# Kernel optimization log

Measured on AMD Instinct MI355X. Metric: run time of the kernel, lower is better.

The kernel has to match this reference:

```python
import jax, jax.numpy as jnp
import numpy as np

B, T, H, V = 16, 400, 400, 22000
S, STEPS, NG = 30, 8, 3  # n_slots, max_res_len, n_gates


def setup_inputs() -> dict:
    key = jax.random.key(0)
    ks = jax.random.split(key, 12)
    r = lambda k, shape, s: jax.random.normal(k, shape, jnp.float32) * s
    lens = jnp.sort(jax.random.randint(ks[8], (B,), T // 2, T + 1))[::-1]
    lens = lens.at[0].set(T)  # torch code only masks up to max(lens); make max(lens)==T
    return {
        "embedding": r(ks[0], (V, H), 0.1),
        "gru_Wih": r(ks[1], (3 * H, H), 0.05),
        "gru_Whh": r(ks[2], (3 * H, H), 0.05),
        "gru_bih": jnp.zeros((3 * H,), jnp.float32),
        "gru_bhh": jnp.zeros((3 * H,), jnp.float32),
        "W_ratio": r(ks[3], (1, 3 * H), 0.05),
        "b_ratio": jnp.zeros((1,), jnp.float32),
        "W_gate": r(ks[4], (NG, H), 0.05),
        "b_gate": jnp.zeros((NG,), jnp.float32),
        "slot_embs": r(ks[5], (S, H), 0.1),  # domain_emb + slot_emb, precombined per domain-slot
        "encoded_hidden": r(ks[6], (B, H), 1.0),
        "encoded_outputs": r(ks[7], (B, T, H), 1.0),
        "encoded_lens": lens,
        "story": jax.random.randint(ks[9], (B, T), 0, V),
        "target_batches": jax.random.randint(ks[10], (B, S, STEPS), 0, V),
    }


def reference(embedding, gru_Wih, gru_Whh, gru_bih, gru_bhh, W_ratio, b_ratio,
              W_gate, b_gate, slot_embs, encoded_hidden, encoded_outputs,
              encoded_lens, story, target_batches):
    # dropout is identity at eval; use_teacher_forcing=True.
    mask = jnp.arange(T)[None, :] < encoded_lens[:, None]          # [B, T]
    batch_idx = jnp.arange(B)[:, None]

    def gru_cell(x, h):
        gi = x @ gru_Wih.T + gru_bih                                # [B, 3H]
        gh = h @ gru_Whh.T + gru_bhh
        i_r, i_z, i_n = jnp.split(gi, 3, axis=-1)
        h_r, h_z, h_n = jnp.split(gh, 3, axis=-1)
        r = jax.nn.sigmoid(i_r + h_r)
        z = jax.nn.sigmoid(i_z + h_z)
        n = jnp.tanh(i_n + r * h_n)
        return (1.0 - z) * n + z * h

    def per_slot(slot_emb, tgt_steps):  # slot_emb [H], tgt_steps [STEPS, B]
        dec_in0 = jnp.broadcast_to(slot_emb[None, :], (B, H))

        def step(carry, tgt_w):
            h, dec_in = carry
            h = gru_cell(dec_in, h)                                 # dec_state == new hidden
            logits = jnp.einsum('bth,bh->bt', encoded_outputs, h)   # [B, T]
            attn = jax.nn.softmax(jnp.where(mask, logits, -1e9), axis=1)
            context = jnp.einsum('bt,bth->bh', attn, encoded_outputs)
            p_vocab = jax.nn.softmax(h @ embedding.T, axis=1)       # [B, V]
            pg_in = jnp.concatenate([h, context, dec_in], axis=-1)  # [B, 3H]
            p_gen = jax.nn.sigmoid(pg_in @ W_ratio.T + b_ratio)     # [B, 1]
            p_ctx = jnp.zeros((B, V), p_vocab.dtype).at[batch_idx, story].add(attn)
            p_final = (1.0 - p_gen) * p_ctx + p_gen * p_vocab       # [B, V]
            dec_next = embedding[tgt_w]                             # teacher forcing
            return (h, dec_next), (p_final, context)

        _, (points, contexts) = jax.lax.scan(step, (encoded_hidden, dec_in0), tgt_steps)
        gate = contexts[0] @ W_gate.T + b_gate                      # gate uses step-0 context
        return jnp.transpose(points, (1, 0, 2)), gate               # [B, STEPS, V], [B, NG]

    targets = jnp.transpose(target_batches, (1, 2, 0))              # [S, STEPS, B]
    all_point_outputs, all_gate_outputs = jax.vmap(per_slot)(slot_embs, targets)
    return all_point_outputs, all_gate_outputs  # [S,B,STEPS,V], [S,B,NG]
```

## Files before the change

kernel.cpp:

```cpp
#include <hip/hip_runtime.h>
#include <hip/hip_bf16.h>

#define DEV __device__ __forceinline__

constexpr int B = 16, T = 400, H = 400, V = 22000, S = 30, STEPS = 8, NG = 3;
constexpr int M  = S * B;
constexpr int H3 = 3 * H;
constexpr int KP = 416;
constexpr int VP = 22016;
constexpr int MP = 512;
constexpr int MR = STEPS * MP;
constexpr int NWP = 1280;
constexpr int NBLK = VP / 128;
constexpr int NMP = MR / 256;
constexpr int NVB = NBLK * NMP;
constexpr int TPAD = 416;
constexpr int PLD = 424;
constexpr long long PTS = (long long)S * B * STEPS * V;

typedef __attribute__((ext_vector_type(8))) short bfrag;
typedef __attribute__((ext_vector_type(4))) float f32x4;
typedef unsigned short u16;

DEV u16 f2bf(float x) {
  unsigned u = __float_as_uint(x);
  u += 0x7FFFu + ((u >> 16) & 1u);
  return (u16)(u >> 16);
}
DEV u16 f2bfn(float x) {
  __hip_bfloat16 h = __float2bfloat16(x);
  union { __hip_bfloat16 b; u16 u; } cv; cv.b = h; return cv.u;
}
DEV float bf2f(u16 h) { return __uint_as_float(((unsigned)h) << 16); }
DEV float sigm(float x) { return 1.0f / (1.0f + __expf(-x)); }

DEV void gload16(const u16* g, u16* l) {
  __builtin_amdgcn_global_load_lds(
      (const __attribute__((address_space(1))) void*)g,
      (__attribute__((address_space(3))) void*)l, 16, 0, 0);
}

constexpr int N_EMB = VP * KP / 256;
constexpr int N_ENC = B * 400 * TPAD / 256;
constexpr int N_W   = NWP * KP / 256;
constexpr int N_DEC = STEPS * MP * KP / 256;
constexpr int N_H0  = MP * KP / 256;
constexpr int N_ZP  = STEPS * (MP - M) * KP / 256;
constexpr int N_ZE  = MR * 16 / 256;
constexpr int N_INIT = N_EMB + N_ENC + N_W + N_DEC + N_H0 + N_ZP + N_ZE;

__global__ __launch_bounds__(256) void k_init(
    const float* __restrict__ emb, const float* __restrict__ enc,
    const float* __restrict__ Wih, const float* __restrict__ Whh,
    const float* __restrict__ semb, const float* __restrict__ ehid,
    const int* __restrict__ tgt,
    u16* __restrict__ ebf, u16* __restrict__ encbK, u16* __restrict__ encT,
    u16* __restrict__ wihH, u16* __restrict__ wihL,
    u16* __restrict__ whhH, u16* __restrict__ whhL,
    float* __restrict__ dec, u16* __restrict__ decH, u16* __restrict__ decL,
    float* __restrict__ h0F, u16* __restrict__ h0H, u16* __restrict__ h0L,
    u16* __restrict__ hAllH, u16* __restrict__ hAllL, u16* __restrict__ ebuf)
{
  int bx = blockIdx.x;
  const int tid = threadIdx.x;
  if (bx < N_EMB) {
    int i = bx * 256 + tid;
    int v = i / KP, k = i % KP;
    ebf[i] = f2bf((v < V && k < H) ? emb[(long long)v * H + k] : 0.f);
    return;
  }
  bx -= N_EMB;
  if (bx < N_ENC) {
    int i = bx * 256 + tid;
    int c = i % TPAD, r = (i / TPAD) % 400, b = i / (TPAD * 400);
    encbK[i] = f2bf((c < H) ? enc[((size_t)b * T + r) * H + c] : 0.f);
    encT[i]  = f2bf((c < T) ? enc[((size_t)b * T + c) * H + r] : 0.f);
    return;
  }
  bx -= N_ENC;
  if (bx < N_W) {
    int i = bx * 256 + tid;
    int n = i / KP, k = i % KP;
    float v1 = (n < H3 && k < H) ? Wih[n * H + k] : 0.f;
    u16 h1 = f2bf(v1);
    wihH[i] = h1; wihL[i] = f2bf(v1 - bf2f(h1));
    float v2 = (n < H3 && k < H) ? Whh[n * H + k] : 0.f;
    u16 h2 = f2bf(v2);
    whhH[i] = h2; whhL[i] = f2bf(v2 - bf2f(h2));
    return;
  }
  bx -= N_W;
  if (bx < N_DEC) {
    int i = bx * 256 + tid;
    int k = i % KP, m = (i / KP) % MP, s = i / (KP * MP);
    float val = 0.f;
    if (m < M && k < H) {
      int slot = m / B, b = m % B;
      if (s == 0) val = semb[slot * H + k];
      else        val = emb[(long long)tgt[(b * S + slot) * STEPS + (s - 1)] * H + k];
      dec[((long long)s * M + m) * H + k] = val;
    }
    u16 hi = f2bf(val);
    decH[i] = hi; decL[i] = f2bf(val - bf2f(hi));
    return;
  }
  bx -= N_DEC;
  if (bx < N_H0) {
    int i = bx * 256 + tid;
    int k = i % KP, m = i / KP;
    float val = (m < M && k < H) ? ehid[(m % B) * H + k] : 0.f;
    if (m < M && k < H) h0F[m * H + k] = val;
    u16 hi = f2bf(val);
    h0H[i] = hi; h0L[i] = f2bf(val - bf2f(hi));
    return;
  }
  bx -= N_H0;
  if (bx < N_ZP) {
    int i = bx * 256 + tid;
    int k = i % KP;
    int row = M + (i / KP) % (MP - M);
    int s = i / (KP * (MP - M));
    size_t idx = ((size_t)s * MP + row) * KP + k;
    hAllH[idx] = 0; hAllL[idx] = 0;
    return;
  }
  bx -= N_ZP;
  {
    int i = bx * 256 + tid;
    int row = i / 16, col = V + (i % 16);
    ebuf[(size_t)row * VP + col] = 0;
  }
}

__global__ __launch_bounds__(256) void k_gemm64s(
    const u16* __restrict__ Ahi, const u16* __restrict__ Alo,
    const u16* __restrict__ Bmh, const u16* __restrict__ Bml,
    const float* __restrict__ bias, float* __restrict__ C,
    int Mvalid, int Nvalid, int Cstride)
{
  __shared__ u16 BsH[64 * 32], BsL[64 * 32];
  const int tid = threadIdx.x;
  const int wave = tid >> 6, lane = tid & 63;
  const int wm = wave >> 1, wn = wave & 1;
  const int n0 = blockIdx.x * 64;
  const int m0 = blockIdx.y * 64;
  const int lrow = lane & 15;
  const int c16 = lane >> 4;
  const int srow = tid >> 2;
  const int sg = (tid & 3) ^ (srow & 3);
  f32x4 acc[2][2] = {};

  const u16* aH = Ahi + (size_t)(m0 + wm * 32 + lrow) * KP + c16 * 8;
  const u16* aL = Alo + (size_t)(m0 + wm * 32 + lrow) * KP + c16 * 8;
  const u16* bHs = Bmh + (size_t)(n0 + srow) * KP + sg * 8;
  const u16* bLs = Bml + (size_t)(n0 + srow) * KP + sg * 8;
  u16* lBH = BsH + wave * 512;
  u16* lBL = BsL + wave * 512;

  for (int kk = 0; kk < KP / 32; ++kk) {
    const int kb = kk * 32;
    gload16(bHs + kb, lBH);
    gload16(bLs + kb, lBL);
    __syncthreads();
    bfrag a0h = *(const bfrag*)(aH + kb);
    bfrag a1h = *(const bfrag*)(aH + 16 * KP + kb);
    bfrag a0l = *(const bfrag*)(aL + kb);
    bfrag a1l = *(const bfrag*)(aL + 16 * KP + kb);
#pragma unroll
    for (int nn = 0; nn < 2; ++nn) {
      const int br = wn * 32 + nn * 16 + lrow;
      const int goff = br * 32 + ((c16 ^ (br & 3)) << 3);
      bfrag bh = *(const bfrag*)&BsH[goff];
      bfrag bl = *(const bfrag*)&BsL[goff];
      acc[0][nn] = __builtin_amdgcn_mfma_f32_16x16x32_bf16(a0h, bh, acc[0][nn], 0, 0, 0);
      acc[1][nn] = __builtin_amdgcn_mfma_f32_16x16x32_bf16(a1h, bh, acc[1][nn], 0, 0, 0);
      acc[0][nn] = __builtin_amdgcn_mfma_f32_16x16x32_bf16(a0h, bl, acc[0][nn], 0, 0, 0);
      acc[1][nn] = __builtin_amdgcn_mfma_f32_16x16x32_bf16(a1h, bl, acc[1][nn], 0, 0, 0);
      acc[0][nn] = __builtin_amdgcn_mfma_f32_16x16x32_bf16(a0l, bh, acc[0][nn], 0, 0, 0);
      acc[1][nn] = __builtin_amdgcn_mfma_f32_16x16x32_bf16(a1l, bh, acc[1][nn], 0, 0, 0);
    }
    __syncthreads();
  }
  const int orow = (lane >> 4) << 2, ocol = lane & 15;
#pragma unroll
  for (int am = 0; am < 2; ++am) {
#pragma unroll
    for (int nn = 0; nn < 2; ++nn) {
      const int gn = n0 + wn * 32 + nn * 16 + ocol;
      if (gn >= Nvalid) continue;
      const float badd = bias[gn];
#pragma unroll
      for (int r = 0; r < 4; ++r) {
        const int gm = m0 + wm * 32 + am * 16 + orow + r;
        if (gm < Mvalid) C[(long long)gm * Cstride + gn] = acc[am][nn][r] + badd;
      }
    }
  }
}

__global__ __launch_bounds__(512) void k_cell(const float* __restrict__ gi_s,
                                              const float* __restrict__ gh,
                                              const float* __restrict__ hprevF,
                                              float* __restrict__ hcurF,
                                              u16* __restrict__ hHc, u16* __restrict__ hLc) {
  int i = blockIdx.x * 512 + threadIdx.x;
  if (i >= M * H) return;
  int k = i % H, m = i / H;
  float ir = gi_s[m * H3 + k],         hr = gh[m * H3 + k];
  float iz = gi_s[m * H3 + H + k],     hz = gh[m * H3 + H + k];
  float in_ = gi_s[m * H3 + 2*H + k],  hn = gh[m * H3 + 2*H + k];
  float rr = sigm(ir + hr);
  float z = sigm(iz + hz);
  float n = tanhf(in_ + rr * hn);
  float hv = (1.f - z) * n + z * hprevF[i];
  hcurF[i] = hv;
  u16 hb = f2bf(hv);
  hHc[m * KP + k] = hb;
  hLc[m * KP + k] = f2bf(hv - bf2f(hb));
}

struct SMatt {
  u16 P[32 * PLD];
  float partm[32][4];
  float parts[32][4];
  float rowred[32];
  float part2[32][4][4];
};

__global__ __launch_bounds__(512) void k_attn(
    const u16* __restrict__ hAllH, const u16* __restrict__ hAllL,
    const float* __restrict__ hallF,
    const u16* __restrict__ encbK, const u16* __restrict__ encT,
    const int* __restrict__ lens, const float* __restrict__ dec,
    const float* __restrict__ Wr, const float* __restrict__ br,
    const float* __restrict__ Wg, const float* __restrict__ bg,
    float* __restrict__ attnB, float* __restrict__ pgenB, float* __restrict__ out)
{
  __shared__ SMatt sm;
  const int s = blockIdx.x >> 4;
  const int b = blockIdx.x & 15;
  const int tid = threadIdx.x;
  const int wave = tid >> 6, lane = tid & 63;
  const int mt = wave & 1;
  const int wg = wave >> 1;
  const int lrow = lane & 15;
  const int c16 = lane >> 4;
  const int len = lens[b];
  const int rbase = mt * 16 + c16 * 4;

  for (int idx = tid; idx < 32 * 24; idx += 512)
    sm.P[(idx / 24) * PLD + 400 + (idx % 24)] = 0;

  f32x4 acc[7] = {};
  {
    const size_t arow = (size_t)s * MP + (size_t)(mt * 16 + lrow) * B + b;
    const u16* aHp = hAllH + arow * KP + c16 * 8;
    const u16* aLp = hAllL + arow * KP + c16 * 8;
    const u16* bBase = encbK + (size_t)b * 400 * TPAD + c16 * 8;
    for (int kk = 0; kk < 13; ++kk) {
      bfrag ah = *(const bfrag*)(aHp + kk * 32);
      bfrag al = *(const bfrag*)(aLp + kk * 32);
#pragma unroll
      for (int i = 0; i < 7; ++i) {
        const int jt = wg + 4 * i;
        if (jt < 25) {
          bfrag bv = *(const bfrag*)(bBase + (size_t)(jt * 16 + lrow) * TPAD + kk * 32);
          acc[i] = __builtin_amdgcn_mfma_f32_16x16x32_bf16(ah, bv, acc[i], 0, 0, 0);
          acc[i] = __builtin_amdgcn_mfma_f32_16x16x32_bf16(al, bv, acc[i], 0, 0, 0);
        }
      }
    }
  }

  {
    float pm[4] = {-1e30f, -1e30f, -1e30f, -1e30f};
#pragma unroll
    for (int i = 0; i < 7; ++i) {
      const int jt = wg + 4 * i;
      if (jt >= 25) continue;
      const int t = jt * 16 + lrow;
      const bool ok = t < len;
#pragma unroll
      for (int rr = 0; rr < 4; ++rr) pm[rr] = fmaxf(pm[rr], ok ? acc[i][rr] : -1e30f);
    }
#pragma unroll
    for (int d = 1; d < 16; d <<= 1) {
#pragma unroll
      for (int rr = 0; rr < 4; ++rr) pm[rr] = fmaxf(pm[rr], __shfl_xor(pm[rr], d));
    }
    if (lrow == 0) {
#pragma unroll
      for (int rr = 0; rr < 4; ++rr) sm.partm[rbase + rr][wg] = pm[rr];
    }
  }
  __syncthreads();
  if (tid < 32)
    sm.rowred[tid] = fmaxf(fmaxf(sm.partm[tid][0], sm.partm[tid][1]),
                           fmaxf(sm.partm[tid][2], sm.partm[tid][3]));
  __syncthreads();
  float Mx[4];
#pragma unroll
  for (int rr = 0; rr < 4; ++rr) Mx[rr] = sm.rowred[rbase + rr];
  {
    float ps[4] = {0.f, 0.f, 0.f, 0.f};
#pragma unroll
    for (int i = 0; i < 7; ++i) {
      const int jt = wg + 4 * i;
      if (jt >= 25) continue;
      const int t = jt * 16 + lrow;
      const bool ok = t < len;
#pragma unroll
      for (int rr = 0; rr < 4; ++rr) {
        float e = ok ? __expf(acc[i][rr] - Mx[rr]) : 0.f;
        acc[i][rr] = e;
        ps[rr] += e;
      }
    }
#pragma unroll
    for (int d = 1; d < 16; d <<= 1) {
#pragma unroll
      for (int rr = 0; rr < 4; ++rr) ps[rr] += __shfl_xor(ps[rr], d);
    }
    if (lrow == 0) {
#pragma unroll
      for (int rr = 0; rr < 4; ++rr) sm.parts[rbase + rr][wg] = ps[rr];
    }
  }
  __syncthreads();
  if (tid < 32)
    sm.rowred[tid] = sm.parts[tid][0] + sm.parts[tid][1] + sm.parts[tid][2] + sm.parts[tid][3];
  __syncthreads();
  {
    float inv[4];
#pragma unroll
    for (int rr = 0; rr < 4; ++rr) inv[rr] = 1.f / sm.rowred[rbase + rr];
#pragma unroll
    for (int i = 0; i < 7; ++i) {
      const int jt = wg + 4 * i;
      if (jt >= 25) continue;
      const int t = jt * 16 + lrow;
#pragma unroll
      for (int rr = 0; rr < 4; ++rr) {
        const int row = rbase + rr;
        const float p = acc[i][rr] * inv[rr];
        sm.P[row * PLD + t] = f2bfn(p);
        if (row < 30) attnB[((size_t)s * M + row * B + b) * T + t] = p;
      }
    }
  }
  __syncthreads();

  f32x4 acc2[7] = {};
  {
    const u16* bBase = encT + (size_t)b * 400 * TPAD + c16 * 8;
    const u16* aP = sm.P + (mt * 16 + lrow) * PLD + c16 * 8;
    for (int kk = 0; kk < 13; ++kk) {
      bfrag ap = *(const bfrag*)(aP + kk * 32);
#pragma unroll
      for (int i = 0; i < 7; ++i) {
        const int jk = wg + 4 * i;
        if (jk < 25) {
          bfrag bv = *(const bfrag*)(bBase + (size_t)(jk * 16 + lrow) * TPAD + kk * 32);
          acc2[i] = __builtin_amdgcn_mfma_f32_16x16x32_bf16(ap, bv, acc2[i], 0, 0, 0);
        }
      }
    }
  }
  {
    float pw[4] = {0.f, 0.f, 0.f, 0.f};
    float pg0[4] = {0.f, 0.f, 0.f, 0.f};
    float pg1[4] = {0.f, 0.f, 0.f, 0.f};
    float pg2[4] = {0.f, 0.f, 0.f, 0.f};
    const bool do_g = (s == 0);
#pragma unroll
    for (int i = 0; i < 7; ++i) {
      const int jk = wg + 4 * i;
      if (jk >= 25) continue;
      const int k = jk * 16 + lrow;
      const float wr = Wr[H + k];
      float w0 = 0.f, w1 = 0.f, w2 = 0.f;
      if (do_g) { w0 = Wg[k]; w1 = Wg[H + k]; w2 = Wg[2 * H + k]; }
#pragma unroll
      for (int rr = 0; rr < 4; ++rr) {
        const float v = acc2[i][rr];
        pw[rr] = fmaf(v, wr, pw[rr]);
        if (do_g) {
          pg0[rr] = fmaf(v, w0, pg0[rr]);
          pg1[rr] = fmaf(v, w1, pg1[rr]);
          pg2[rr] = fmaf(v, w2, pg2[rr]);
        }
      }
    }
#pragma unroll
    for (int d = 1; d < 16; d <<= 1) {
#pragma unroll
      for (int rr = 0; rr < 4; ++rr) {
        pw[rr] += __shfl_xor(pw[rr], d);
        pg0[rr] += __shfl_xor(pg0[rr], d);
        pg1[rr] += __shfl_xor(pg1[rr], d);
        pg2[rr] += __shfl_xor(pg2[rr], d);
      }
    }
    if (lrow == 0) {
#pragma unroll
      for (int rr = 0; rr < 4; ++rr) {
        sm.part2[rbase + rr][wg][0] = pw[rr];
        sm.part2[rbase + rr][wg][1] = pg0[rr];
        sm.part2[rbase + rr][wg][2] = pg1[rr];
        sm.part2[rbase + rr][wg][3] = pg2[rr];
      }
    }
  }
  __syncthreads();

  if (tid < 480) {
    const int row = tid >> 4;
    const int l16 = tid & 15;
    const int m = row * B + b;
    const float* hF = hallF + ((size_t)s * M + m) * H;
    const float* dF = dec + ((size_t)s * M + m) * H;
    float p = 0.f;
    for (int j = 0; j < 25; ++j) {
      const int k = l16 + 16 * j;
      p += hF[k] * Wr[k] + dF[k] * Wr[2 * H + k];
    }
#pragma unroll
    for (int d = 1; d < 16; d <<= 1) p += __shfl_xor(p, d);
    if (l16 == 0) {
      float cw = sm.part2[row][0][0] + sm.part2[row][1][0] +
                 sm.part2[row][2][0] + sm.part2[row][3][0];
      pgenB[s * M + m] = sigm(p + cw + br[0]);
    }
    if (s == 0 && l16 < NG) {
      float gv = sm.part2[row][0][1 + l16] + sm.part2[row][1][1 + l16] +
                 sm.part2[row][2][1 + l16] + sm.part2[row][3][1 + l16];
      out[PTS + (long long)m * NG + l16] = gv + bg[l16];
    }
  }
}

__global__ __launch_bounds__(512) void k_vocab(
    const u16* __restrict__ hAllH, const u16* __restrict__ ebf,
    u16* __restrict__ ebuf)
{
  __shared__ u16 Bs[4][4096];
  const int bx = blockIdx.x;
  const int tid = threadIdx.x;
  const int wave = tid >> 6, lane = tid & 63;
  const int bxs = (bx & 7) * (NVB / 8) + (bx >> 3);
  const int nb = bxs / NMP;
  const int mp = bxs % NMP;
  const int n0 = nb * 128;
  const int m0 = mp * 256;
  const int wm = wave >> 1, wn = wave & 1;
  const int lrow = lane & 15;
  const int c16 = lane >> 4;
  const int srow = tid >> 2;
  const int sg = (tid & 3) ^ (srow & 3);
  f32x4 acc[4][4] = {};

  const u16* aBase = hAllH + (size_t)(m0 + wm * 64 + lrow) * KP + c16 * 8;
  const u16* bS = ebf + (size_t)(n0 + srow) * KP + sg * 8;

  gload16(bS + 0,  &Bs[0][wave * 512]);
  gload16(bS + 32, &Bs[1][wave * 512]);
  int cur = 0;
#pragma unroll 1
  for (int p = 0; p < 7; ++p) {
    const int kb = p * 64;
    bfrag a[4][2];
#pragma unroll
    for (int r = 0; r < 4; ++r) {
      a[r][0] = *(const bfrag*)(aBase + r * 16 * KP + kb);
      if (p < 6) a[r][1] = *(const bfrag*)(aBase + r * 16 * KP + kb + 32);
    }
    if (p < 5) {
      gload16(bS + kb + 64, &Bs[(cur ^ 1) * 2 + 0][wave * 512]);
      gload16(bS + kb + 96, &Bs[(cur ^ 1) * 2 + 1][wave * 512]);
      asm volatile("s_waitcnt vmcnt(10)" ::: "memory");
    } else if (p == 5) {
      gload16(bS + kb + 64, &Bs[(cur ^ 1) * 2 + 0][wave * 512]);
      asm volatile("s_waitcnt vmcnt(9)" ::: "memory");
    } else {
      asm volatile("s_waitcnt vmcnt(4)" ::: "memory");
    }
    __builtin_amdgcn_sched_barrier(0);
    __builtin_amdgcn_s_barrier();
    {
      const u16* Bb = Bs[cur * 2 + 0];
      bfrag bfv[4];
#pragma unroll
      for (int nn = 0; nn < 4; ++nn) {
        const int brr = wn * 64 + nn * 16 + lrow;
        bfv[nn] = *(const bfrag*)&Bb[brr * 32 + ((c16 ^ (brr & 3)) << 3)];
      }
#pragma unroll
      for (int nn = 0; nn < 4; ++nn) {
#pragma unroll
        for (int r = 0; r < 4; ++r)
          acc[r][nn] = __builtin_amdgcn_mfma_f32_16x16x32_bf16(a[r][0], bfv[nn], acc[r][nn], 0, 0, 0);
      }
    }
    if (p < 6) {
      const u16* Bb = Bs[cur * 2 + 1];
      bfrag bfv[4];
#pragma unroll
      for (int nn = 0; nn < 4; ++nn) {
        const int brr = wn * 64 + nn * 16 + lrow;
        bfv[nn] = *(const bfrag*)&Bb[brr * 32 + ((c16 ^ (brr & 3)) << 3)];
      }
#pragma unroll
      for (int nn = 0; nn < 4; ++nn) {
#pragma unroll
        for (int r = 0; r < 4; ++r)
          acc[r][nn] = __builtin_amdgcn_mfma_f32_16x16x32_bf16(a[r][1], bfv[nn], acc[r][nn], 0, 0, 0);
      }
    }
    __builtin_amdgcn_sched_barrier(0);
    __builtin_amdgcn_s_barrier();
    __builtin_amdgcn_sched_barrier(0);
    cur ^= 1;
  }

  const int orow = (lane >> 4) << 2, ocol = lane & 15;
#pragma unroll
  for (int af = 0; af < 4; ++af) {
#pragma unroll
    for (int r = 0; r < 4; ++r) {
      const int rl = wm * 64 + af * 16 + orow + r;
      const size_t R = (size_t)m0 + rl;
      if ((R % MP) >= M) continue;
#pragma unroll
      for (int nn = 0; nn < 4; ++nn) {
        const int gn = n0 + wn * 64 + nn * 16 + ocol;
        if (gn < V) ebuf[R * VP + gn] = f2bfn(__expf(acc[af][nn][r]));
      }
    }
  }
}

__global__ __launch_bounds__(512) void k_merge(
    const u16* __restrict__ ebuf, const float* __restrict__ pgenB,
    const float* __restrict__ attnB, const int* __restrict__ story,
    float* __restrict__ out)
{
  const int bxi = blockIdx.x;
  const int s = bxi / M, m = bxi % M, b = m % B;
  const size_t R = (size_t)s * MP + m;
  const int tid = threadIdx.x;
  const int wave = tid >> 6, lane = tid & 63;
  __shared__ float red8[8];
  const u16* erow = ebuf + R * VP;
  bfrag ch[6];
  float sum = 0.f;
#pragma unroll
  for (int j = 0; j < 6; ++j) {
    const int c = j * 512 + tid;
    if (c < VP / 8) {
      ch[j] = *(const bfrag*)(erow + (size_t)c * 8);
#pragma unroll
      for (int e = 0; e < 8; ++e) sum += bf2f((u16)ch[j][e]);
    }
  }
#pragma unroll
  for (int off = 32; off; off >>= 1) sum += __shfl_xor(sum, off);
  if (lane == 0) red8[wave] = sum;
  __syncthreads();
  float Sv = 0.f;
#pragma unroll
  for (int j = 0; j < 8; ++j) Sv += red8[j];
  const float pg = pgenB[s * M + m];
  const float scale = pg / Sv;
  float* orow = out + ((size_t)m * STEPS + s) * V;
#pragma unroll
  for (int j = 0; j < 6; ++j) {
    const int c = j * 512 + tid;
    if (c < V / 8) {
      f32x4 w0, w1;
#pragma unroll
      for (int e = 0; e < 4; ++e) {
        w0[e] = bf2f((u16)ch[j][e]) * scale;
        w1[e] = bf2f((u16)ch[j][4 + e]) * scale;
      }
      *(f32x4*)(orow + (size_t)c * 8) = w0;
      *(f32x4*)(orow + (size_t)c * 8 + 4) = w1;
    }
  }
  __syncthreads();
  const float om = 1.f - pg;
  for (int t = tid; t < T; t += 512) {
    float a = attnB[((size_t)s * M + m) * T + t];
    if (a != 0.f) atomicAdd(orow + story[b * T + t], om * a);
  }
}


extern "C" void kernel_launch(void* const* d_in, const int* in_sizes, int n_in,
                              void* d_out, int out_size, void* d_ws, size_t ws_size,
                              hipStream_t stream) {
  (void)in_sizes; (void)n_in; (void)out_size; (void)ws_size;
  const float* emb  = (const float*)d_in[0];
  const float* Wih  = (const float*)d_in[1];
  const float* Whh  = (const float*)d_in[2];
  const float* bih  = (const float*)d_in[3];
  const float* bhh  = (const float*)d_in[4];
  const float* Wr   = (const float*)d_in[5];
  const float* br   = (const float*)d_in[6];
  const float* Wg   = (const float*)d_in[7];
  const float* bg   = (const float*)d_in[8];
  const float* semb = (const float*)d_in[9];
  const float* ehid = (const float*)d_in[10];
  const float* enc  = (const float*)d_in[11];
  const int*   lens = (const int*)d_in[12];
  const int*   story= (const int*)d_in[13];
  const int*   tgt  = (const int*)d_in[14];
  float* out = (float*)d_out;

  char* w = (char*)d_ws;
  size_t off = 0;
  auto alloc = [&](size_t n) -> void* {
    void* p = w + off;
    off = (off + n + 255) & ~(size_t)255;
    return p;
  };
  u16* ebf    = (u16*)alloc((size_t)VP * KP * 2);
  u16* wihH   = (u16*)alloc((size_t)NWP * KP * 2);
  u16* wihL   = (u16*)alloc((size_t)NWP * KP * 2);
  u16* whhH   = (u16*)alloc((size_t)NWP * KP * 2);
  u16* whhL   = (u16*)alloc((size_t)NWP * KP * 2);
  u16* decH   = (u16*)alloc((size_t)STEPS * MP * KP * 2);
  u16* decL   = (u16*)alloc((size_t)STEPS * MP * KP * 2);
  float* dec  = (float*)alloc((size_t)STEPS * M * H * 4);
  float* h0F  = (float*)alloc((size_t)M * H * 4);
  u16* h0H    = (u16*)alloc((size_t)MP * KP * 2);
  u16* h0L    = (u16*)alloc((size_t)MP * KP * 2);
  u16* hAllH  = (u16*)alloc((size_t)MR * KP * 2);
  u16* hAllL  = (u16*)alloc((size_t)MR * KP * 2);
  float* hallF= (float*)alloc((size_t)STEPS * M * H * 4);
  float* gi   = (float*)alloc((size_t)MR * H3 * 4);
  float* gh   = (float*)alloc((size_t)M * H3 * 4);
  float* attnB= (float*)alloc((size_t)STEPS * M * T * 4);
  float* pgenB= (float*)alloc((size_t)STEPS * M * 4);
  u16* ebuf   = (u16*)alloc((size_t)MR * VP * 2);
  u16* encbK  = (u16*)alloc((size_t)B * 400 * TPAD * 2);
  u16* encT   = (u16*)alloc((size_t)B * 400 * TPAD * 2);

  k_init<<<N_INIT, 256, 0, stream>>>(emb, enc, Wih, Whh, semb, ehid, tgt,
      ebf, encbK, encT, wihH, wihL, whhH, whhL, dec, decH, decL,
      h0F, h0H, h0L, hAllH, hAllL, ebuf);
  k_gemm64s<<<dim3((H3 + 63) / 64, MR / 64), 256, 0, stream>>>(
      decH, decL, wihH, wihL, bih, gi, MR, H3, H3);

  for (int s = 0; s < STEPS; ++s) {
    const u16* pH = (s == 0) ? h0H : hAllH + (size_t)(s - 1) * MP * KP;
    const u16* pL = (s == 0) ? h0L : hAllL + (size_t)(s - 1) * MP * KP;
    const float* pF = (s == 0) ? h0F : hallF + (size_t)(s - 1) * M * H;
    k_gemm64s<<<dim3((H3 + 63) / 64, (M + 63) / 64), 256, 0, stream>>>(
        pH, pL, whhH, whhL, bhh, gh, M, H3, H3);
    k_cell<<<(M * H + 511) / 512, 512, 0, stream>>>(
        gi + (size_t)s * MP * H3, gh, pF,
        hallF + (size_t)s * M * H,
        hAllH + (size_t)s * MP * KP, hAllL + (size_t)s * MP * KP);
  }

  k_vocab<<<NVB, 512, 0, stream>>>(hAllH, ebf, ebuf);
  k_attn<<<STEPS * B, 512, 0, stream>>>(hAllH, hAllL, hallF, encbK, encT, lens,
                                        dec, Wr, br, Wg, bg, attnB, pgenB, out);
  k_merge<<<STEPS * M, 512, 0, stream>>>(ebuf, pgenB, attnB, story, out);
}
```

Before: 605.1 us.

## Fuse per-step vocab GEMM with recurrent GEMM to overlap serial GRU chain

Splits the single large vocab-projection GEMM into per-step slices and launches each slice in the same kernel as the next step's recurrent h@Whh GEMM. Block index decides which role a block takes, so the vocab work fills the GPU while the small, latency-bound recurrent GEMM runs. This removes the separate vocab kernel at the end and hides it behind the sequential GRU loop. In exchange the recurrent GEMM now runs with 512-thread blocks of which half idle, and per-step vocab launches have smaller grids with less L2 reuse of the embedding matrix.

```diff
diff --git a/kernel.cpp b/kernel.cpp
--- a/kernel.cpp
+++ b/kernel.cpp
@@ -14,6 +14,9 @@
 constexpr int NBLK = VP / 128;
 constexpr int NMP = MR / 256;
 constexpr int NVB = NBLK * NMP;
+constexpr int NVB_S = NBLK * 2;
+constexpr int NCT = (H3 + 63) / 64;
+constexpr int NGH = NCT * ((M + 63) / 64);
 constexpr int TPAD = 416;
 constexpr int PLD = 424;
 constexpr long long PTS = (long long)S * B * STEPS * V;
@@ -217,6 +220,177 @@
   u16 hb = f2bf(hv);
   hHc[m * KP + k] = hb;
   hLc[m * KP + k] = f2bf(hv - bf2f(hb));
+}
+
+__global__ __launch_bounds__(512) void k_bigv(
+    const u16* __restrict__ hPrevH, const u16* __restrict__ hPrevL,
+    const u16* __restrict__ ebf, u16* __restrict__ ebuf, long long Rbase,
+    const u16* __restrict__ whhH, const u16* __restrict__ whhL,
+    const float* __restrict__ bhh, float* __restrict__ gh)
+{
+  __shared__ union SMU {
+    u16 vb[4][4096];
+    struct { u16 bh[64 * 32]; u16 bl[64 * 32]; } g;
+  } sm;
+  const int bx = blockIdx.x;
+  const int tid = threadIdx.x;
+  const int wave = tid >> 6, lane = tid & 63;
+
+  if (bx < NVB_S) {
+    const int bxs = (bx & 7) * (NVB_S / 8) + (bx >> 3);
+    const int nb = bxs >> 1;
+    const int m0 = (bxs & 1) * 256;
+    const int n0 = nb * 128;
+    const int wm = wave >> 1, wn = wave & 1;
+    const int lrow = lane & 15;
+    const int c16 = lane >> 4;
+    const int srow = tid >> 2;
+    const int sg = (tid & 3) ^ (srow & 3);
+    f32x4 acc[4][4] = {};
+
+    const u16* aBase = hPrevH + (size_t)(m0 + wm * 64 + lrow) * KP + c16 * 8;
+    const u16* bS = ebf + (size_t)(n0 + srow) * KP + sg * 8;
+
+    gload16(bS + 0,  &sm.vb[0][wave * 512]);
+    gload16(bS + 32, &sm.vb[1][wave * 512]);
+    int cur = 0;
+#pragma unroll 1
+    for (int p = 0; p < 7; ++p) {
+      const int kb = p * 64;
+      bfrag a[4][2];
+#pragma unroll
+      for (int r = 0; r < 4; ++r) {
+        a[r][0] = *(const bfrag*)(aBase + r * 16 * KP + kb);
+        if (p < 6) a[r][1] = *(const bfrag*)(aBase + r * 16 * KP + kb + 32);
+      }
+      if (p < 5) {
+        gload16(bS + kb + 64, &sm.vb[(cur ^ 1) * 2 + 0][wave * 512]);
+        gload16(bS + kb + 96, &sm.vb[(cur ^ 1) * 2 + 1][wave * 512]);
+        asm volatile("s_waitcnt vmcnt(10)" ::: "memory");
+      } else if (p == 5) {
+        gload16(bS + kb + 64, &sm.vb[(cur ^ 1) * 2 + 0][wave * 512]);
+        asm volatile("s_waitcnt vmcnt(9)" ::: "memory");
+      } else {
+        asm volatile("s_waitcnt vmcnt(4)" ::: "memory");
+      }
+      __builtin_amdgcn_sched_barrier(0);
+      __builtin_amdgcn_s_barrier();
+      {
+        const u16* Bb = sm.vb[cur * 2 + 0];
+        bfrag bfv[4];
+#pragma unroll
+        for (int nn = 0; nn < 4; ++nn) {
+          const int brr = wn * 64 + nn * 16 + lrow;
+          bfv[nn] = *(const bfrag*)&Bb[brr * 32 + ((c16 ^ (brr & 3)) << 3)];
+        }
+#pragma unroll
+        for (int nn = 0; nn < 4; ++nn) {
+#pragma unroll
+          for (int r = 0; r < 4; ++r)
+            acc[r][nn] = __builtin_amdgcn_mfma_f32_16x16x32_bf16(a[r][0], bfv[nn], acc[r][nn], 0, 0, 0);
+        }
+      }
+      if (p < 6) {
+        const u16* Bb = sm.vb[cur * 2 + 1];
+        bfrag bfv[4];
+#pragma unroll
+        for (int nn = 0; nn < 4; ++nn) {
+          const int brr = wn * 64 + nn * 16 + lrow;
+          bfv[nn] = *(const bfrag*)&Bb[brr * 32 + ((c16 ^ (brr & 3)) << 3)];
+        }
+#pragma unroll
+        for (int nn = 0; nn < 4; ++nn) {
+#pragma unroll
+          for (int r = 0; r < 4; ++r)
+            acc[r][nn] = __builtin_amdgcn_mfma_f32_16x16x32_bf16(a[r][1], bfv[nn], acc[r][nn], 0, 0, 0);
+        }
+      }
+      __builtin_amdgcn_sched_barrier(0);
+      __builtin_amdgcn_s_barrier();
+      __builtin_amdgcn_sched_barrier(0);
+      cur ^= 1;
+    }
+
+    const int orow = (lane >> 4) << 2, ocol = lane & 15;
+#pragma unroll
+    for (int af = 0; af < 4; ++af) {
+#pragma unroll
+      for (int r = 0; r < 4; ++r) {
+        const int rl = m0 + wm * 64 + af * 16 + orow + r;
+        if (rl >= M) continue;
+        const size_t R = (size_t)(Rbase + rl);
+#pragma unroll
+        for (int nn = 0; nn < 4; ++nn) {
+          const int gn = n0 + wn * 64 + nn * 16 + ocol;
+          if (gn < V) ebuf[R * VP + gn] = f2bfn(__expf(acc[af][nn][r]));
+        }
+      }
+    }
+  } else {
+    const int gb = bx - NVB_S;
+    const int n0 = (gb % NCT) * 64;
+    const int m0 = (gb / NCT) * 64;
+    const bool act = tid < 256;
+    const int wm = wave >> 1, wn = wave & 1;
+    const int lrow = lane & 15;
+    const int c16 = lane >> 4;
+    const int srow = tid >> 2;
+    const int sg = (tid & 3) ^ (srow & 3);
+    f32x4 acc[2][2] = {};
+
+    const u16* aH = hPrevH + (size_t)(m0 + (wm & 1) * 32 + lrow) * KP + c16 * 8;
+    const u16* aL = hPrevL + (size_t)(m0 + (wm & 1) * 32 + lrow) * KP + c16 * 8;
+    const u16* bHs = whhH + (size_t)(n0 + (srow & 63)) * KP + sg * 8;
+    const u16* bLs = whhL + (size_t)(n0 + (srow & 63)) * KP + sg * 8;
+    u16* lBH = sm.g.bh + (wave & 3) * 512;
+    u16* lBL = sm.g.bl + (wave & 3) * 512;
+
+    for (int kk = 0; kk < KP / 32; ++kk) {
+      const int kb = kk * 32;
+      if (act) {
+        gload16(bHs + kb, lBH);
+        gload16(bLs + kb, lBL);
+      }
+      __syncthreads();
+      if (act) {
+        bfrag a0h = *(const bfrag*)(aH + kb);
+        bfrag a1h = *(const bfrag*)(aH + 16 * KP + kb);
+        bfrag a0l = *(const bfrag*)(aL + kb);
+        bfrag a1l = *(const bfrag*)(aL + 16 * KP + kb);
+#pragma unroll
+        for (int nn = 0; nn < 2; ++nn) {
+          const int br = wn * 32 + nn * 16 + lrow;
+          const int goff = br * 32 + ((c16 ^ (br & 3)) << 3);
+          bfrag bh = *(const bfrag*)&sm.g.bh[goff];
+          bfrag bl = *(const bfrag*)&sm.g.bl[goff];
+          acc[0][nn] = __builtin_amdgcn_mfma_f32_16x16x32_bf16(a0h, bh, acc[0][nn], 0, 0, 0);
+          acc[1][nn] = __builtin_amdgcn_mfma_f32_16x16x32_bf16(a1h, bh, acc[1][nn], 0, 0, 0);
+          acc[0][nn] = __builtin_amdgcn_mfma_f32_16x16x32_bf16(a0h, bl, acc[0][nn], 0, 0, 0);
+          acc[1][nn] = __builtin_amdgcn_mfma_f32_16x16x32_bf16(a1h, bl, acc[1][nn], 0, 0, 0);
+          acc[0][nn] = __builtin_amdgcn_mfma_f32_16x16x32_bf16(a0l, bh, acc[0][nn], 0, 0, 0);
+          acc[1][nn] = __builtin_amdgcn_mfma_f32_16x16x32_bf16(a1l, bh, acc[1][nn], 0, 0, 0);
+        }
+      }
+      __syncthreads();
+    }
+    if (act) {
+      const int orow = (lane >> 4) << 2, ocol = lane & 15;
+#pragma unroll
+      for (int am = 0; am < 2; ++am) {
+#pragma unroll
+        for (int nn = 0; nn < 2; ++nn) {
+          const int gn = n0 + wn * 32 + nn * 16 + ocol;
+          if (gn >= H3) continue;
+          const float badd = bhh[gn];
+#pragma unroll
+          for (int r = 0; r < 4; ++r) {
+            const int gm = m0 + wm * 32 + am * 16 + orow + r;
+            if (gm < M) gh[(long long)gm * H3 + gn] = acc[am][nn][r] + badd;
+          }
+        }
+      }
+    }
+  }
 }
 
 struct SMatt {
@@ -435,106 +609,6 @@
       float gv = sm.part2[row][0][1 + l16] + sm.part2[row][1][1 + l16] +
                  sm.part2[row][2][1 + l16] + sm.part2[row][3][1 + l16];
       out[PTS + (long long)m * NG + l16] = gv + bg[l16];
-    }
-  }
-}
-
-__global__ __launch_bounds__(512) void k_vocab(
-    const u16* __restrict__ hAllH, const u16* __restrict__ ebf,
-    u16* __restrict__ ebuf)
-{
-  __shared__ u16 Bs[4][4096];
-  const int bx = blockIdx.x;
-  const int tid = threadIdx.x;
-  const int wave = tid >> 6, lane = tid & 63;
-  const int bxs = (bx & 7) * (NVB / 8) + (bx >> 3);
-  const int nb = bxs / NMP;
-  const int mp = bxs % NMP;
-  const int n0 = nb * 128;
-  const int m0 = mp * 256;
-  const int wm = wave >> 1, wn = wave & 1;
-  const int lrow = lane & 15;
-  const int c16 = lane >> 4;
-  const int srow = tid >> 2;
-  const int sg = (tid & 3) ^ (srow & 3);
-  f32x4 acc[4][4] = {};
-
-  const u16* aBase = hAllH + (size_t)(m0 + wm * 64 + lrow) * KP + c16 * 8;
-  const u16* bS = ebf + (size_t)(n0 + srow) * KP + sg * 8;
-
-  gload16(bS + 0,  &Bs[0][wave * 512]);
-  gload16(bS + 32, &Bs[1][wave * 512]);
-  int cur = 0;
-#pragma unroll 1
-  for (int p = 0; p < 7; ++p) {
-    const int kb = p * 64;
-    bfrag a[4][2];
-#pragma unroll
-    for (int r = 0; r < 4; ++r) {
-      a[r][0] = *(const bfrag*)(aBase + r * 16 * KP + kb);
-      if (p < 6) a[r][1] = *(const bfrag*)(aBase + r * 16 * KP + kb + 32);
-    }
-    if (p < 5) {
-      gload16(bS + kb + 64, &Bs[(cur ^ 1) * 2 + 0][wave * 512]);
-      gload16(bS + kb + 96, &Bs[(cur ^ 1) * 2 + 1][wave * 512]);
-      asm volatile("s_waitcnt vmcnt(10)" ::: "memory");
-    } else if (p == 5) {
-      gload16(bS + kb + 64, &Bs[(cur ^ 1) * 2 + 0][wave * 512]);
-      asm volatile("s_waitcnt vmcnt(9)" ::: "memory");
-    } else {
-      asm volatile("s_waitcnt vmcnt(4)" ::: "memory");
-    }
-    __builtin_amdgcn_sched_barrier(0);
-    __builtin_amdgcn_s_barrier();
-    {
-      const u16* Bb = Bs[cur * 2 + 0];
-      bfrag bfv[4];
-#pragma unroll
-      for (int nn = 0; nn < 4; ++nn) {
-        const int brr = wn * 64 + nn * 16 + lrow;
-        bfv[nn] = *(const bfrag*)&Bb[brr * 32 + ((c16 ^ (brr & 3)) << 3)];
-      }
-#pragma unroll
-      for (int nn = 0; nn < 4; ++nn) {
-#pragma unroll
-        for (int r = 0; r < 4; ++r)
-          acc[r][nn] = __builtin_amdgcn_mfma_f32_16x16x32_bf16(a[r][0], bfv[nn], acc[r][nn], 0, 0, 0);
-      }
-    }
-    if (p < 6) {
-      const u16* Bb = Bs[cur * 2 + 1];
-      bfrag bfv[4];
-#pragma unroll
-      for (int nn = 0; nn < 4; ++nn) {
-        const int brr = wn * 64 + nn * 16 + lrow;
-        bfv[nn] = *(const bfrag*)&Bb[brr * 32 + ((c16 ^ (brr & 3)) << 3)];
-      }
-#pragma unroll
-      for (int nn = 0; nn < 4; ++nn) {
-#pragma unroll
-        for (int r = 0; r < 4; ++r)
-          acc[r][nn] = __builtin_amdgcn_mfma_f32_16x16x32_bf16(a[r][1], bfv[nn], acc[r][nn], 0, 0, 0);
-      }
-    }
-    __builtin_amdgcn_sched_barrier(0);
-    __builtin_amdgcn_s_barrier();
-    __builtin_amdgcn_sched_barrier(0);
-    cur ^= 1;
-  }
-
-  const int orow = (lane >> 4) << 2, ocol = lane & 15;
-#pragma unroll
-  for (int af = 0; af < 4; ++af) {
-#pragma unroll
-    for (int r = 0; r < 4; ++r) {
-      const int rl = wm * 64 + af * 16 + orow + r;
-      const size_t R = (size_t)m0 + rl;
-      if ((R % MP) >= M) continue;
-#pragma unroll
-      for (int nn = 0; nn < 4; ++nn) {
-        const int gn = n0 + wn * 64 + nn * 16 + ocol;
-        if (gn < V) ebuf[R * VP + gn] = f2bfn(__expf(acc[af][nn][r]));
-      }
     }
   }
 }
@@ -648,22 +722,27 @@
   k_init<<<N_INIT, 256, 0, stream>>>(emb, enc, Wih, Whh, semb, ehid, tgt,
       ebf, encbK, encT, wihH, wihL, whhH, whhL, dec, decH, decL,
       h0F, h0H, h0L, hAllH, hAllL, ebuf);
-  k_gemm64s<<<dim3((H3 + 63) / 64, MR / 64), 256, 0, stream>>>(
+  k_gemm64s<<<dim3(NCT, MR / 64), 256, 0, stream>>>(
       decH, decL, wihH, wihL, bih, gi, MR, H3, H3);
 
-  for (int s = 0; s < STEPS; ++s) {
-    const u16* pH = (s == 0) ? h0H : hAllH + (size_t)(s - 1) * MP * KP;
-    const u16* pL = (s == 0) ? h0L : hAllL + (size_t)(s - 1) * MP * KP;
-    const float* pF = (s == 0) ? h0F : hallF + (size_t)(s - 1) * M * H;
-    k_gemm64s<<<dim3((H3 + 63) / 64, (M + 63) / 64), 256, 0, stream>>>(
-        pH, pL, whhH, whhL, bhh, gh, M, H3, H3);
+  k_gemm64s<<<dim3(NCT, (M + 63) / 64), 256, 0, stream>>>(
+      h0H, h0L, whhH, whhL, bhh, gh, M, H3, H3);
+  k_cell<<<(M * H + 511) / 512, 512, 0, stream>>>(
+      gi, gh, h0F, hallF, hAllH, hAllL);
+
+  for (int s = 1; s < STEPS; ++s) {
+    k_bigv<<<NVB_S + NGH, 512, 0, stream>>>(
+        hAllH + (size_t)(s - 1) * MP * KP, hAllL + (size_t)(s - 1) * MP * KP,
+        ebf, ebuf, (long long)(s - 1) * MP, whhH, whhL, bhh, gh);
     k_cell<<<(M * H + 511) / 512, 512, 0, stream>>>(
-        gi + (size_t)s * MP * H3, gh, pF,
+        gi + (size_t)s * MP * H3, gh, hallF + (size_t)(s - 1) * M * H,
         hallF + (size_t)s * M * H,
         hAllH + (size_t)s * MP * KP, hAllL + (size_t)s * MP * KP);
   }
-
-  k_vocab<<<NVB, 512, 0, stream>>>(hAllH, ebf, ebuf);
+  k_bigv<<<NVB_S, 512, 0, stream>>>(
+      hAllH + (size_t)7 * MP * KP, hAllL + (size_t)7 * MP * KP,
+      ebf, ebuf, (long long)7 * MP, whhH, whhL, bhh, gh);
+
   k_attn<<<STEPS * B, 512, 0, stream>>>(hAllH, hAllL, hallF, encbK, encT, lens,
                                         dec, Wr, br, Wg, bg, attnB, pgenB, out);
   k_merge<<<STEPS * M, 512, 0, stream>>>(ebuf, pgenB, attnB, story, out);
```

Result: faster. 554.5 us (-8.4%).
